# Kernel tuning notes

Measured on AMD Instinct MI355X. Metric: run time of the kernel, lower is better.

The kernel has to match this reference:

```python
import jax, jax.numpy as jnp
import numpy as np

N_NODES = 50000
N_EDGES = 800000
D_FEAT = 128


def setup_inputs() -> dict:
    key = jax.random.key(0)
    k1, k2, k3, k4 = jax.random.split(key, 4)
    edge_index = jax.random.randint(k1, (2, N_EDGES), 0, N_NODES, dtype=jnp.int64 if jax.config.jax_enable_x64 else jnp.int32)
    edge_vals = jax.random.uniform(k2, (N_EDGES,), dtype=jnp.float32)
    features = jax.random.normal(k3, (N_NODES, D_FEAT), dtype=jnp.float32)
    bias = jax.random.normal(k4, (D_FEAT,), dtype=jnp.float32)
    return {"edge_index": edge_index, "edge_vals": edge_vals, "features": features, "bias": bias}


def reference(edge_index, edge_vals, features, bias):
    # SpMM: out[dst] += A[dst, src] * X[src], i.e. sparse adjacency @ dense features
    src = edge_index[0]
    dst = edge_index[1]
    msg = features[src] * edge_vals[:, None]          # [E, D] gather + scale
    out = jax.ops.segment_sum(msg, dst, num_segments=features.shape[0])  # [N, D] scatter-add
    return out + bias                                  # fused bias add
```

## Files before the change

kernel.cpp:

```cpp
#include <hip/hip_runtime.h>
#include <hip/hip_bf16.h>

#define D_FEAT 128
#define D4 (D_FEAT / 4)
#define BKT_SHIFT 7
#define BKT_NODES 128
#define NCHUNK 256
#define MAXBKT 512
#define MAXBSUM 128
#define CAP 3072

__device__ inline unsigned pack_bf2(float lo, float hi) {
    __hip_bfloat162 h = __float22bfloat162_rn(make_float2(lo, hi));
    unsigned u;
    __builtin_memcpy(&u, &h, 4);
    return u;
}

__global__ __launch_bounds__(256) void k1_hist_cvt(
        const int* __restrict__ dst, int E, int chunk, int nbkt,
        int* __restrict__ M, int Mpad,
        const float4* __restrict__ fin, uint2* __restrict__ fout,
        int n4) {
    int c = blockIdx.x;
    int tid = threadIdx.x;
    if (c < NCHUNK) {
        __shared__ int hist[MAXBKT];
        for (int i = tid; i < nbkt; i += 256) hist[i] = 0;
        __syncthreads();
        int lo = c * chunk;
        int hi = min(lo + chunk, E);
        for (int i = lo + tid; i < hi; i += 256)
            atomicAdd(&hist[dst[i] >> BKT_SHIFT], 1);
        __syncthreads();
        for (int i = tid; i < nbkt; i += 256)
            M[i * NCHUNK + c] = hist[i];
        if (c == 0) {
            for (int i = nbkt * NCHUNK + tid; i < Mpad; i += 256) M[i] = 0;
        }
    } else {
        int nb = gridDim.x - NCHUNK;
        int idx = (c - NCHUNK) * 256 + tid;
        int stride = nb * 256;
        for (int i = idx; i < n4; i += stride) {
            float4 f = fin[i];
            uint2 o;
            o.x = pack_bf2(f.x, f.y);
            o.y = pack_bf2(f.z, f.w);
            fout[i] = o;
        }
    }
}

__global__ __launch_bounds__(1024) void k2a_scan(int* __restrict__ M,
                                                 int* __restrict__ bsum) {
    __shared__ int s[1024];
    int tid = threadIdx.x;
    int j = blockIdx.x * 1024 + tid;
    int v = M[j];
    s[tid] = v;
    __syncthreads();
    for (int off = 1; off < 1024; off <<= 1) {
        int t = (tid >= off) ? s[tid - off] : 0;
        __syncthreads();
        s[tid] += t;
        __syncthreads();
    }
    M[j] = s[tid] - v;
    if (tid == 1023) bsum[blockIdx.x] = s[1023];
}

__device__ inline void scan_bsum_wave(const int* __restrict__ bsum, int nblk,
                                      int* sbs, int tid) {
    if (tid < 64) {
        int i0 = 2 * tid, i1 = 2 * tid + 1;
        int h0 = (i0 < nblk) ? bsum[i0] : 0;
        int h1 = (i1 < nblk) ? bsum[i1] : 0;
        int s = h0 + h1;
        int v = s;
        for (int off = 1; off < 64; off <<= 1) {
            int t = __shfl_up(v, off, 64);
            if (tid >= off) v += t;
        }
        sbs[i0] = v - s;
        sbs[i1] = v - s + h0;
    }
    __syncthreads();
}

__global__ __launch_bounds__(512) void k3_partition(
        const int* __restrict__ src, const int* __restrict__ dst,
        const float* __restrict__ vals, int E, int chunk, int nbkt, int nblk,
        const int* __restrict__ M, const int* __restrict__ bsum,
        int2* __restrict__ spackA) {
    __shared__ int sbs[MAXBSUM];
    __shared__ int lcur[MAXBKT];
    int c = blockIdx.x;
    int tid = threadIdx.x;
    scan_bsum_wave(bsum, nblk, sbs, tid);
    for (int i = tid; i < nbkt; i += 512) {
        int j = i * NCHUNK + c;
        lcur[i] = M[j] + sbs[j >> 10];
    }
    __syncthreads();
    int lo = c * chunk;
    int hi = min(lo + chunk, E);
    for (int i = lo + tid; i < hi; i += 512) {
        int d = dst[i];
        int s = src[i];
        float v = vals[i];
        int pos = atomicAdd(&lcur[d >> BKT_SHIFT], 1);
        spackA[pos] = make_int2((s & 0xFFFF) | ((d & (BKT_NODES - 1)) << 16),
                                __float_as_int(v));
    }
}

__global__ __launch_bounds__(1024) void k45_sort_gather(
        const int* __restrict__ M, const int* __restrict__ bsum, int nblk,
        const int2* __restrict__ spackA, int2* __restrict__ spackB,
        const uint2* __restrict__ feat2,
        const float4* __restrict__ bias4, float4* __restrict__ out4,
        int N, int nbkt) {
    __shared__ int sbs[MAXBSUM];
    __shared__ int hist[BKT_NODES];
    __shared__ int sbuf[BKT_NODES];
    __shared__ int lcur[BKT_NODES];
    __shared__ int2 ls[CAP];
    int b = blockIdx.x;
    int tid = threadIdx.x;
    scan_bsum_wave(bsum, nblk, sbs, tid);
    int j0 = b * NCHUNK;
    int j1 = (b + 1) * NCHUNK;
    int base = M[j0] + sbs[j0 >> 10];
    int end  = M[j1] + sbs[j1 >> 10];
    int cnt = end - base;
    bool inlds = (cnt <= CAP);

    if (tid < BKT_NODES) hist[tid] = 0;
    __syncthreads();
    for (int i = tid; i < cnt; i += 1024)
        atomicAdd(&hist[(spackA[base + i].x >> 16) & (BKT_NODES - 1)], 1);
    __syncthreads();
    if (tid < 64) {
        int h0 = hist[2 * tid], h1 = hist[2 * tid + 1];
        int s = h0 + h1;
        int v = s;
        for (int off = 1; off < 64; off <<= 1) {
            int t = __shfl_up(v, off, 64);
            if (tid >= off) v += t;
        }
        sbuf[2 * tid]     = v - h1;
        sbuf[2 * tid + 1] = v;
        lcur[2 * tid]     = v - s;
        lcur[2 * tid + 1] = v - h1;
    }
    __syncthreads();
    for (int i = tid; i < cnt; i += 1024) {
        int2 r = spackA[base + i];
        int p = atomicAdd(&lcur[(r.x >> 16) & (BKT_NODES - 1)], 1);
        if (inlds) ls[p] = r;
        else       spackB[base + p] = r;
    }
    __syncthreads();

    int wave = tid >> 6, lane = tid & 63;
    int half = lane >> 5;
    int hl   = lane & 31;
    float4 bv = bias4[hl];
    for (int n = wave; n < BKT_NODES; n += 16) {
        int node = (b << BKT_SHIFT) + n;
        if (node >= N) break;
        int lend = sbuf[n];
        int lbeg = lend - hist[n];
        float4 acc0 = make_float4(0.f, 0.f, 0.f, 0.f);
        float4 acc1 = make_float4(0.f, 0.f, 0.f, 0.f);
        if (inlds) {
            for (int e0 = lbeg; e0 < lend; e0 += 16) {
                int2 p[8];
                uint2 h[8];
#pragma unroll
                for (int j = 0; j < 8; j++)
                    p[j] = ls[min(e0 + 2 * j + half, lend - 1)];
#pragma unroll
                for (int j = 0; j < 8; j++)
                    h[j] = feat2[(size_t)(p[j].x & 0xFFFF) * 32 + hl];
#pragma unroll
                for (int j = 0; j < 8; j++) {
                    float v = (e0 + 2 * j + half < lend) ? __int_as_float(p[j].y) : 0.f;
                    __hip_bfloat162 blo, bhi;
                    __builtin_memcpy(&blo, &h[j].x, 4);
                    __builtin_memcpy(&bhi, &h[j].y, 4);
                    float2 f01 = __bfloat1622float2(blo);
                    float2 f23 = __bfloat1622float2(bhi);
                    if (j & 1) {
                        acc1.x += v * f01.x; acc1.y += v * f01.y;
                        acc1.z += v * f23.x; acc1.w += v * f23.y;
                    } else {
                        acc0.x += v * f01.x; acc0.y += v * f01.y;
                        acc0.z += v * f23.x; acc0.w += v * f23.y;
                    }
                }
            }
        } else {
            for (int e0 = lbeg; e0 < lend; e0 += 16) {
                int2 p[8];
                uint2 h[8];
#pragma unroll
                for (int j = 0; j < 8; j++)
                    p[j] = spackB[base + min(e0 + 2 * j + half, lend - 1)];
#pragma unroll
                for (int j = 0; j < 8; j++)
                    h[j] = feat2[(size_t)(p[j].x & 0xFFFF) * 32 + hl];
#pragma unroll
                for (int j = 0; j < 8; j++) {
                    float v = (e0 + 2 * j + half < lend) ? __int_as_float(p[j].y) : 0.f;
                    __hip_bfloat162 blo, bhi;
                    __builtin_memcpy(&blo, &h[j].x, 4);
                    __builtin_memcpy(&bhi, &h[j].y, 4);
                    float2 f01 = __bfloat1622float2(blo);
                    float2 f23 = __bfloat1622float2(bhi);
                    if (j & 1) {
                        acc1.x += v * f01.x; acc1.y += v * f01.y;
                        acc1.z += v * f23.x; acc1.w += v * f23.y;
                    } else {
                        acc0.x += v * f01.x; acc0.y += v * f01.y;
                        acc0.z += v * f23.x; acc0.w += v * f23.y;
                    }
                }
            }
        }
        acc0.x += acc1.x; acc0.y += acc1.y;
        acc0.z += acc1.z; acc0.w += acc1.w;
        acc0.x += __shfl_xor(acc0.x, 32);
        acc0.y += __shfl_xor(acc0.y, 32);
        acc0.z += __shfl_xor(acc0.z, 32);
        acc0.w += __shfl_xor(acc0.w, 32);
        if (half == 0) {
            out4[(size_t)node * 32 + hl] =
                make_float4(acc0.x + bv.x, acc0.y + bv.y,
                            acc0.z + bv.z, acc0.w + bv.w);
        }
    }
}


__global__ void init_bias_kernel(float4* __restrict__ out,
                                 const float4* __restrict__ bias, int n4) {
    int i = blockIdx.x * blockDim.x + threadIdx.x;
    if (i < n4) out[i] = bias[i & (D4 - 1)];
}

__global__ void spmm_edge_kernel(const int* __restrict__ src,
                                 const int* __restrict__ dst,
                                 const float* __restrict__ vals,
                                 const float4* __restrict__ feat,
                                 float* __restrict__ out, int n_edges) {
    int tid = blockIdx.x * blockDim.x + threadIdx.x;
    int e = tid >> 5;
    int lane = tid & 31;
    if (e >= n_edges) return;
    int s = src[e];
    int d = dst[e];
    float v = vals[e];
    float4 f = feat[(size_t)s * D4 + lane];
    float* o = out + (size_t)d * D_FEAT + lane * 4;
    atomicAdd(o + 0, v * f.x);
    atomicAdd(o + 1, v * f.y);
    atomicAdd(o + 2, v * f.z);
    atomicAdd(o + 3, v * f.w);
}

extern "C" void kernel_launch(void* const* d_in, const int* in_sizes, int n_in,
                              void* d_out, int out_size, void* d_ws, size_t ws_size,
                              hipStream_t stream) {
    const int* edge_index = (const int*)d_in[0];
    const float* edge_vals = (const float*)d_in[1];
    const float* features  = (const float*)d_in[2];
    const float* bias      = (const float*)d_in[3];

    int E = in_sizes[1];
    int N = in_sizes[2] / D_FEAT;
    const int* src = edge_index;
    const int* dst = edge_index + E;
    float* out = (float*)d_out;

    int nbkt = (N + BKT_NODES - 1) >> BKT_SHIFT;
    int n4 = N * D_FEAT / 4;
    int chunk = (E + NCHUNK - 1) / NCHUNK;
    int Mpad = ((nbkt * NCHUNK + 1 + 1023) / 1024) * 1024;
    int nblk2 = Mpad / 1024;

    size_t fb_bytes = (size_t)N * D_FEAT * 2;
    size_t sp_bytes = (size_t)E * 8;
    size_t needed = fb_bytes + 2 * sp_bytes +
                    ((size_t)Mpad + nblk2) * 4;

    bool ok = (ws_size >= needed) && (N >= 1) && (N <= 65536) && (E >= 1) &&
              (in_sizes[3] == D_FEAT) && (nbkt <= MAXBKT) && (nblk2 <= MAXBSUM);

    if (ok) {
        char* wp = (char*)d_ws;
        uint2* fb16 = (uint2*)wp;                      wp += fb_bytes;
        int2* spackA = (int2*)wp;                      wp += sp_bytes;
        int2* spackB = (int2*)wp;                      wp += sp_bytes;
        int* M       = (int*)wp;                       wp += (size_t)Mpad * 4;
        int* bsum    = (int*)wp;

        k1_hist_cvt<<<NCHUNK + 256, 256, 0, stream>>>(dst, E, chunk, nbkt,
                                                      M, Mpad,
                                                      (const float4*)features,
                                                      fb16, n4);
        k2a_scan<<<nblk2, 1024, 0, stream>>>(M, bsum);
        k3_partition<<<NCHUNK, 512, 0, stream>>>(src, dst, edge_vals, E, chunk,
                                                 nbkt, nblk2, M, bsum, spackA);
        k45_sort_gather<<<nbkt, 1024, 0, stream>>>(M, bsum, nblk2,
                                                   spackA, spackB,
                                                   (const uint2*)fb16,
                                                   (const float4*)bias,
                                                   (float4*)out, N, nbkt);
    } else {
        int no4 = out_size / 4;
        {
            int block = 256, grid = (no4 + block - 1) / block;
            init_bias_kernel<<<grid, block, 0, stream>>>((float4*)out,
                                                         (const float4*)bias, no4);
        }
        {
            int block = 256;
            long long total = (long long)E * 32;
            int grid = (int)((total + block - 1) / block);
            spmm_edge_kernel<<<grid, block, 0, stream>>>(src, dst, edge_vals,
                                                         (const float4*)features,
                                                         out, E);
        }
    }
}
```

Baseline: 144.1 us.

## Fuse histogram, scan, partition and sort-gather into one cooperative persistent kernel

Replaces the four-kernel pipeline with a single cooperative launch that uses grid-wide syncs between the histogram/convert, scan, partition and bucket sort-gather phases. Blocks loop over chunks and buckets in a persistent style. The goal is to remove the launch gaps and tail drains between kernels. In exchange, grid size is capped by occupancy: 1024-thread blocks with large LDS use fewer blocks per CU, so phases such as the 256-chunk partition and 391-bucket gather may serialise. Grid syncs also cost time.

```diff
diff --git a/kernel.cpp b/kernel.cpp
--- a/kernel.cpp
+++ b/kernel.cpp
@@ -1,5 +1,8 @@
 #include <hip/hip_runtime.h>
 #include <hip/hip_bf16.h>
+#include <hip/hip_cooperative_groups.h>
+
+namespace cg = cooperative_groups;
 
 #define D_FEAT 128
 #define D4 (D_FEAT / 4)
@@ -15,59 +18,6 @@
     unsigned u;
     __builtin_memcpy(&u, &h, 4);
     return u;
-}
-
-__global__ __launch_bounds__(256) void k1_hist_cvt(
-        const int* __restrict__ dst, int E, int chunk, int nbkt,
-        int* __restrict__ M, int Mpad,
-        const float4* __restrict__ fin, uint2* __restrict__ fout,
-        int n4) {
-    int c = blockIdx.x;
-    int tid = threadIdx.x;
-    if (c < NCHUNK) {
-        __shared__ int hist[MAXBKT];
-        for (int i = tid; i < nbkt; i += 256) hist[i] = 0;
-        __syncthreads();
-        int lo = c * chunk;
-        int hi = min(lo + chunk, E);
-        for (int i = lo + tid; i < hi; i += 256)
-            atomicAdd(&hist[dst[i] >> BKT_SHIFT], 1);
-        __syncthreads();
-        for (int i = tid; i < nbkt; i += 256)
-            M[i * NCHUNK + c] = hist[i];
-        if (c == 0) {
-            for (int i = nbkt * NCHUNK + tid; i < Mpad; i += 256) M[i] = 0;
-        }
-    } else {
-        int nb = gridDim.x - NCHUNK;
-        int idx = (c - NCHUNK) * 256 + tid;
-        int stride = nb * 256;
-        for (int i = idx; i < n4; i += stride) {
-            float4 f = fin[i];
-            uint2 o;
-            o.x = pack_bf2(f.x, f.y);
-            o.y = pack_bf2(f.z, f.w);
-            fout[i] = o;
-        }
-    }
-}
-
-__global__ __launch_bounds__(1024) void k2a_scan(int* __restrict__ M,
-                                                 int* __restrict__ bsum) {
-    __shared__ int s[1024];
-    int tid = threadIdx.x;
-    int j = blockIdx.x * 1024 + tid;
-    int v = M[j];
-    s[tid] = v;
-    __syncthreads();
-    for (int off = 1; off < 1024; off <<= 1) {
-        int t = (tid >= off) ? s[tid - off] : 0;
-        __syncthreads();
-        s[tid] += t;
-        __syncthreads();
-    }
-    M[j] = s[tid] - v;
-    if (tid == 1023) bsum[blockIdx.x] = s[1023];
 }
 
 __device__ inline void scan_bsum_wave(const int* __restrict__ bsum, int nblk,
@@ -86,6 +36,260 @@
         sbs[i1] = v - s + h0;
     }
     __syncthreads();
+}
+
+__global__ __launch_bounds__(1024) void fused_all(
+        const int* __restrict__ src, const int* __restrict__ dst,
+        const float* __restrict__ vals, int E, int chunk,
+        int nbkt, int Mpad, int nblk2,
+        int* __restrict__ M, int* __restrict__ bsum,
+        int2* __restrict__ spackA, int2* __restrict__ spackB,
+        const float4* __restrict__ fin4, uint2* __restrict__ fb16, int n4,
+        const float4* __restrict__ bias4, float4* __restrict__ out4, int N) {
+    cg::grid_group grid = cg::this_grid();
+    __shared__ int sh_hist[MAXBKT];
+    __shared__ int sh_scan[1024];
+    __shared__ int sbs[MAXBSUM];
+    __shared__ int lcur[MAXBKT];
+    __shared__ int h4[BKT_NODES];
+    __shared__ int sb4[BKT_NODES];
+    __shared__ int lc4[BKT_NODES];
+    __shared__ int2 ls[CAP];
+    int b = blockIdx.x;
+    int tid = threadIdx.x;
+    int G = gridDim.x;
+
+    for (int c = b; c < NCHUNK; c += G) {
+        for (int i = tid; i < nbkt; i += 1024) sh_hist[i] = 0;
+        __syncthreads();
+        int lo = c * chunk;
+        int hi = min(lo + chunk, E);
+        for (int i = lo + tid; i < hi; i += 1024)
+            atomicAdd(&sh_hist[dst[i] >> BKT_SHIFT], 1);
+        __syncthreads();
+        for (int i = tid; i < nbkt; i += 1024) M[i * NCHUNK + c] = sh_hist[i];
+        __syncthreads();
+    }
+    {
+        int g0 = b * 1024 + tid;
+        for (int i = nbkt * NCHUNK + g0; i < Mpad; i += G * 1024) M[i] = 0;
+        for (int i = g0; i < n4; i += G * 1024) {
+            float4 f = fin4[i];
+            uint2 o;
+            o.x = pack_bf2(f.x, f.y);
+            o.y = pack_bf2(f.z, f.w);
+            fb16[i] = o;
+        }
+    }
+    grid.sync();
+
+    for (int blk = b; blk < nblk2; blk += G) {
+        int j = blk * 1024 + tid;
+        int v = M[j];
+        sh_scan[tid] = v;
+        __syncthreads();
+        for (int off = 1; off < 1024; off <<= 1) {
+            int t = (tid >= off) ? sh_scan[tid - off] : 0;
+            __syncthreads();
+            sh_scan[tid] += t;
+            __syncthreads();
+        }
+        M[j] = sh_scan[tid] - v;
+        if (tid == 1023) bsum[blk] = sh_scan[1023];
+        __syncthreads();
+    }
+    grid.sync();
+
+    scan_bsum_wave(bsum, nblk2, sbs, tid);
+    for (int c = b; c < NCHUNK; c += G) {
+        for (int i = tid; i < nbkt; i += 1024) {
+            int j = i * NCHUNK + c;
+            lcur[i] = M[j] + sbs[j >> 10];
+        }
+        __syncthreads();
+        int lo = c * chunk;
+        int hi = min(lo + chunk, E);
+        for (int i = lo + tid; i < hi; i += 1024) {
+            int d = dst[i];
+            int pos = atomicAdd(&lcur[d >> BKT_SHIFT], 1);
+            spackA[pos] = make_int2((src[i] & 0xFFFF) |
+                                    ((d & (BKT_NODES - 1)) << 16),
+                                    __float_as_int(vals[i]));
+        }
+        __syncthreads();
+    }
+    grid.sync();
+
+    for (int bk = b; bk < nbkt; bk += G) {
+        int j0 = bk * NCHUNK;
+        int j1 = (bk + 1) * NCHUNK;
+        int base = M[j0] + sbs[j0 >> 10];
+        int end  = M[j1] + sbs[j1 >> 10];
+        int cnt = end - base;
+        bool inlds = (cnt <= CAP);
+
+        if (tid < BKT_NODES) h4[tid] = 0;
+        __syncthreads();
+        for (int i = tid; i < cnt; i += 1024)
+            atomicAdd(&h4[(spackA[base + i].x >> 16) & (BKT_NODES - 1)], 1);
+        __syncthreads();
+        if (tid < 64) {
+            int h0 = h4[2 * tid], h1 = h4[2 * tid + 1];
+            int s = h0 + h1;
+            int v = s;
+            for (int off = 1; off < 64; off <<= 1) {
+                int t = __shfl_up(v, off, 64);
+                if (tid >= off) v += t;
+            }
+            sb4[2 * tid]     = v - h1;
+            sb4[2 * tid + 1] = v;
+            lc4[2 * tid]     = v - s;
+            lc4[2 * tid + 1] = v - h1;
+        }
+        __syncthreads();
+        for (int i = tid; i < cnt; i += 1024) {
+            int2 r = spackA[base + i];
+            int p = atomicAdd(&lc4[(r.x >> 16) & (BKT_NODES - 1)], 1);
+            if (inlds) ls[p] = r;
+            else       spackB[base + p] = r;
+        }
+        __syncthreads();
+
+        int wave = tid >> 6, lane = tid & 63;
+        int half = lane >> 5;
+        int hl   = lane & 31;
+        float4 bv = bias4[hl];
+        for (int n = wave; n < BKT_NODES; n += 16) {
+            int node = (bk << BKT_SHIFT) + n;
+            if (node >= N) break;
+            int lend = sb4[n];
+            int lbeg = lend - h4[n];
+            float4 a0 = make_float4(0.f, 0.f, 0.f, 0.f);
+            float4 a1 = make_float4(0.f, 0.f, 0.f, 0.f);
+            if (inlds) {
+                for (int e0 = lbeg; e0 < lend; e0 += 16) {
+                    int2 p[8];
+                    uint2 h[8];
+#pragma unroll
+                    for (int j = 0; j < 8; j++)
+                        p[j] = ls[min(e0 + 2 * j + half, lend - 1)];
+#pragma unroll
+                    for (int j = 0; j < 8; j++)
+                        h[j] = fb16[(size_t)(p[j].x & 0xFFFF) * 32 + hl];
+#pragma unroll
+                    for (int j = 0; j < 8; j++) {
+                        float v = (e0 + 2 * j + half < lend) ?
+                                  __int_as_float(p[j].y) : 0.f;
+                        __hip_bfloat162 blo, bhi;
+                        __builtin_memcpy(&blo, &h[j].x, 4);
+                        __builtin_memcpy(&bhi, &h[j].y, 4);
+                        float2 f01 = __bfloat1622float2(blo);
+                        float2 f23 = __bfloat1622float2(bhi);
+                        if (j & 1) {
+                            a1.x += v * f01.x; a1.y += v * f01.y;
+                            a1.z += v * f23.x; a1.w += v * f23.y;
+                        } else {
+                            a0.x += v * f01.x; a0.y += v * f01.y;
+                            a0.z += v * f23.x; a0.w += v * f23.y;
+                        }
+                    }
+                }
+            } else {
+                for (int e0 = lbeg; e0 < lend; e0 += 16) {
+                    int2 p[8];
+                    uint2 h[8];
+#pragma unroll
+                    for (int j = 0; j < 8; j++)
+                        p[j] = spackB[base + min(e0 + 2 * j + half, lend - 1)];
+#pragma unroll
+                    for (int j = 0; j < 8; j++)
+                        h[j] = fb16[(size_t)(p[j].x & 0xFFFF) * 32 + hl];
+#pragma unroll
+                    for (int j = 0; j < 8; j++) {
+                        float v = (e0 + 2 * j + half < lend) ?
+                                  __int_as_float(p[j].y) : 0.f;
+                        __hip_bfloat162 blo, bhi;
+                        __builtin_memcpy(&blo, &h[j].x, 4);
+                        __builtin_memcpy(&bhi, &h[j].y, 4);
+                        float2 f01 = __bfloat1622float2(blo);
+                        float2 f23 = __bfloat1622float2(bhi);
+                        if (j & 1) {
+                            a1.x += v * f01.x; a1.y += v * f01.y;
+                            a1.z += v * f23.x; a1.w += v * f23.y;
+                        } else {
+                            a0.x += v * f01.x; a0.y += v * f01.y;
+                            a0.z += v * f23.x; a0.w += v * f23.y;
+                        }
+                    }
+                }
+            }
+            a0.x += a1.x; a0.y += a1.y; a0.z += a1.z; a0.w += a1.w;
+            a0.x += __shfl_xor(a0.x, 32);
+            a0.y += __shfl_xor(a0.y, 32);
+            a0.z += __shfl_xor(a0.z, 32);
+            a0.w += __shfl_xor(a0.w, 32);
+            if (half == 0) {
+                out4[(size_t)node * 32 + hl] =
+                    make_float4(a0.x + bv.x, a0.y + bv.y,
+                                a0.z + bv.z, a0.w + bv.w);
+            }
+        }
+        __syncthreads();
+    }
+}
+
+
+__global__ __launch_bounds__(256) void k1_hist_cvt(
+        const int* __restrict__ dst, int E, int chunk, int nbkt,
+        int* __restrict__ M, int Mpad,
+        const float4* __restrict__ fin, uint2* __restrict__ fout,
+        int n4) {
+    int c = blockIdx.x;
+    int tid = threadIdx.x;
+    if (c < NCHUNK) {
+        __shared__ int hist[MAXBKT];
+        for (int i = tid; i < nbkt; i += 256) hist[i] = 0;
+        __syncthreads();
+        int lo = c * chunk;
+        int hi = min(lo + chunk, E);
+        for (int i = lo + tid; i < hi; i += 256)
+            atomicAdd(&hist[dst[i] >> BKT_SHIFT], 1);
+        __syncthreads();
+        for (int i = tid; i < nbkt; i += 256)
+            M[i * NCHUNK + c] = hist[i];
+        if (c == 0) {
+            for (int i = nbkt * NCHUNK + tid; i < Mpad; i += 256) M[i] = 0;
+        }
+    } else {
+        int nb = gridDim.x - NCHUNK;
+        int idx = (c - NCHUNK) * 256 + tid;
+        int stride = nb * 256;
+        for (int i = idx; i < n4; i += stride) {
+            float4 f = fin[i];
+            uint2 o;
+            o.x = pack_bf2(f.x, f.y);
+            o.y = pack_bf2(f.z, f.w);
+            fout[i] = o;
+        }
+    }
+}
+
+__global__ __launch_bounds__(1024) void k2a_scan(int* __restrict__ M,
+                                                 int* __restrict__ bsum) {
+    __shared__ int s[1024];
+    int tid = threadIdx.x;
+    int j = blockIdx.x * 1024 + tid;
+    int v = M[j];
+    s[tid] = v;
+    __syncthreads();
+    for (int off = 1; off < 1024; off <<= 1) {
+        int t = (tid >= off) ? s[tid - off] : 0;
+        __syncthreads();
+        s[tid] += t;
+        __syncthreads();
+    }
+    M[j] = s[tid] - v;
+    if (tid == 1023) bsum[blockIdx.x] = s[1023];
 }
 
 __global__ __launch_bounds__(512) void k3_partition(
@@ -107,11 +311,9 @@
     int hi = min(lo + chunk, E);
     for (int i = lo + tid; i < hi; i += 512) {
         int d = dst[i];
-        int s = src[i];
-        float v = vals[i];
         int pos = atomicAdd(&lcur[d >> BKT_SHIFT], 1);
-        spackA[pos] = make_int2((s & 0xFFFF) | ((d & (BKT_NODES - 1)) << 16),
-                                __float_as_int(v));
+        spackA[pos] = make_int2((src[i] & 0xFFFF) | ((d & (BKT_NODES - 1)) << 16),
+                                __float_as_int(vals[i]));
     }
 }
 
@@ -172,8 +374,8 @@
         if (node >= N) break;
         int lend = sbuf[n];
         int lbeg = lend - hist[n];
-        float4 acc0 = make_float4(0.f, 0.f, 0.f, 0.f);
-        float4 acc1 = make_float4(0.f, 0.f, 0.f, 0.f);
+        float4 a0 = make_float4(0.f, 0.f, 0.f, 0.f);
+        float4 a1 = make_float4(0.f, 0.f, 0.f, 0.f);
         if (inlds) {
             for (int e0 = lbeg; e0 < lend; e0 += 16) {
                 int2 p[8];
@@ -193,11 +395,11 @@
                     float2 f01 = __bfloat1622float2(blo);
                     float2 f23 = __bfloat1622float2(bhi);
                     if (j & 1) {
-                        acc1.x += v * f01.x; acc1.y += v * f01.y;
-                        acc1.z += v * f23.x; acc1.w += v * f23.y;
+                        a1.x += v * f01.x; a1.y += v * f01.y;
+                        a1.z += v * f23.x; a1.w += v * f23.y;
                     } else {
-                        acc0.x += v * f01.x; acc0.y += v * f01.y;
-                        acc0.z += v * f23.x; acc0.w += v * f23.y;
+                        a0.x += v * f01.x; a0.y += v * f01.y;
+                        a0.z += v * f23.x; a0.w += v * f23.y;
                     }
                 }
             }
@@ -220,25 +422,24 @@
                     float2 f01 = __bfloat1622float2(blo);
                     float2 f23 = __bfloat1622float2(bhi);
                     if (j & 1) {
-                        acc1.x += v * f01.x; acc1.y += v * f01.y;
-                        acc1.z += v * f23.x; acc1.w += v * f23.y;
+                        a1.x += v * f01.x; a1.y += v * f01.y;
+                        a1.z += v * f23.x; a1.w += v * f23.y;
                     } else {
-                        acc0.x += v * f01.x; acc0.y += v * f01.y;
-                        acc0.z += v * f23.x; acc0.w += v * f23.y;
+                        a0.x += v * f01.x; a0.y += v * f01.y;
+                        a0.z += v * f23.x; a0.w += v * f23.y;
                     }
                 }
             }
         }
-        acc0.x += acc1.x; acc0.y += acc1.y;
-        acc0.z += acc1.z; acc0.w += acc1.w;
-        acc0.x += __shfl_xor(acc0.x, 32);
-        acc0.y += __shfl_xor(acc0.y, 32);
-        acc0.z += __shfl_xor(acc0.z, 32);
-        acc0.w += __shfl_xor(acc0.w, 32);
+        a0.x += a1.x; a0.y += a1.y; a0.z += a1.z; a0.w += a1.w;
+        a0.x += __shfl_xor(a0.x, 32);
+        a0.y += __shfl_xor(a0.y, 32);
+        a0.z += __shfl_xor(a0.z, 32);
+        a0.w += __shfl_xor(a0.w, 32);
         if (half == 0) {
             out4[(size_t)node * 32 + hl] =
-                make_float4(acc0.x + bv.x, acc0.y + bv.y,
-                            acc0.z + bv.z, acc0.w + bv.w);
+                make_float4(a0.x + bv.x, a0.y + bv.y,
+                            a0.z + bv.z, a0.w + bv.w);
         }
     }
 }
@@ -292,8 +493,7 @@
 
     size_t fb_bytes = (size_t)N * D_FEAT * 2;
     size_t sp_bytes = (size_t)E * 8;
-    size_t needed = fb_bytes + 2 * sp_bytes +
-                    ((size_t)Mpad + nblk2) * 4;
+    size_t needed = fb_bytes + 2 * sp_bytes + ((size_t)Mpad + nblk2) * 4;
 
     bool ok = (ws_size >= needed) && (N >= 1) && (N <= 65536) && (E >= 1) &&
               (in_sizes[3] == D_FEAT) && (nbkt <= MAXBKT) && (nblk2 <= MAXBSUM);
@@ -306,18 +506,53 @@
         int* M       = (int*)wp;                       wp += (size_t)Mpad * 4;
         int* bsum    = (int*)wp;
 
-        k1_hist_cvt<<<NCHUNK + 256, 256, 0, stream>>>(dst, E, chunk, nbkt,
-                                                      M, Mpad,
-                                                      (const float4*)features,
-                                                      fb16, n4);
-        k2a_scan<<<nblk2, 1024, 0, stream>>>(M, bsum);
-        k3_partition<<<NCHUNK, 512, 0, stream>>>(src, dst, edge_vals, E, chunk,
-                                                 nbkt, nblk2, M, bsum, spackA);
-        k45_sort_gather<<<nbkt, 1024, 0, stream>>>(M, bsum, nblk2,
-                                                   spackA, spackB,
-                                                   (const uint2*)fb16,
-                                                   (const float4*)bias,
-                                                   (float4*)out, N, nbkt);
+        static int s_cap = -2;
+        if (s_cap == -2) {
+            int nb = 0;
+            if (hipOccupancyMaxActiveBlocksPerMultiprocessor(
+                    &nb, fused_all, 1024, 0) != hipSuccess) nb = 0;
+            int cus = 0;
+            hipDeviceProp_t prop;
+            int dev = 0;
+            if (hipGetDevice(&dev) == hipSuccess &&
+                hipGetDeviceProperties(&prop, dev) == hipSuccess)
+                cus = prop.multiProcessorCount;
+            s_cap = (nb > 0 && cus > 0) ? nb * cus : 0;
+        }
+
+        bool launched = false;
+        if (s_cap >= 64) {
+            int G = s_cap < 512 ? s_cap : 512;
+            const float4* fin4 = (const float4*)features;
+            const float4* bias4 = (const float4*)bias;
+            float4* out4 = (float4*)out;
+            void* args[] = {
+                (void*)&src, (void*)&dst, (void*)&edge_vals, (void*)&E,
+                (void*)&chunk, (void*)&nbkt, (void*)&Mpad, (void*)&nblk2,
+                (void*)&M, (void*)&bsum, (void*)&spackA, (void*)&spackB,
+                (void*)&fin4, (void*)&fb16, (void*)&n4,
+                (void*)&bias4, (void*)&out4, (void*)&N };
+            hipError_t err = hipLaunchCooperativeKernel(
+                fused_all, dim3(G), dim3(1024), args, 0, stream);
+            if (err == hipSuccess) launched = true;
+            else s_cap = 0;
+        }
+
+        if (!launched) {
+            k1_hist_cvt<<<NCHUNK + 256, 256, 0, stream>>>(dst, E, chunk, nbkt,
+                                                          M, Mpad,
+                                                          (const float4*)features,
+                                                          fb16, n4);
+            k2a_scan<<<nblk2, 1024, 0, stream>>>(M, bsum);
+            k3_partition<<<NCHUNK, 512, 0, stream>>>(src, dst, edge_vals, E,
+                                                     chunk, nbkt, nblk2,
+                                                     M, bsum, spackA);
+            k45_sort_gather<<<nbkt, 1024, 0, stream>>>(M, bsum, nblk2,
+                                                       spackA, spackB,
+                                                       (const uint2*)fb16,
+                                                       (const float4*)bias,
+                                                       (float4*)out, N, nbkt);
+        }
     } else {
         int no4 = out_size / 4;
         {
```

Result: no change. 142.5 us (-1.1%).

## Replace scan-based partition with fixed bucket slots and an overflow path

Applied to the files above, without the earlier changes.

Drops the global histogram matrix, its prefix-scan kernel and the separate partition pass. Each chunk now reserves space in a fixed-size per-bucket slot with a global atomic cursor and scatters edges in the same kernel as the bf16 conversion, which cuts the launch count and removes one full pass over dst. Edges that overflow a slot go to a side list, and a separate kernel adds them into the output with fp32 atomics. This adds a memset, a third launch that always runs, and nondeterministic atomic ordering for overflowed edges.

```diff
diff --git a/kernel.cpp b/kernel.cpp
--- a/kernel.cpp
+++ b/kernel.cpp
@@ -7,8 +7,7 @@
 #define BKT_NODES 128
 #define NCHUNK 256
 #define MAXBKT 512
-#define MAXBSUM 128
-#define CAP 3072
+#define SLOT 5120
 
 __device__ inline unsigned pack_bf2(float lo, float hi) {
     __hip_bfloat162 h = __float22bfloat162_rn(make_float2(lo, hi));
@@ -17,124 +16,71 @@
     return u;
 }
 
-__global__ __launch_bounds__(256) void k1_hist_cvt(
-        const int* __restrict__ dst, int E, int chunk, int nbkt,
-        int* __restrict__ M, int Mpad,
-        const float4* __restrict__ fin, uint2* __restrict__ fout,
-        int n4) {
+__global__ __launch_bounds__(512) void ka_part_cvt(
+        const int* __restrict__ src, const int* __restrict__ dst,
+        const float* __restrict__ vals, int E, int chunk, int nbkt,
+        int* __restrict__ gcur, int* __restrict__ ovcnt, int4* __restrict__ ov,
+        int2* __restrict__ spackA,
+        const float4* __restrict__ fin4, uint2* __restrict__ fb16, int n4) {
     int c = blockIdx.x;
     int tid = threadIdx.x;
     if (c < NCHUNK) {
         __shared__ int hist[MAXBKT];
-        for (int i = tid; i < nbkt; i += 256) hist[i] = 0;
+        __shared__ int lcur[MAXBKT];
+        for (int i = tid; i < nbkt; i += 512) hist[i] = 0;
         __syncthreads();
         int lo = c * chunk;
         int hi = min(lo + chunk, E);
-        for (int i = lo + tid; i < hi; i += 256)
+        for (int i = lo + tid; i < hi; i += 512)
             atomicAdd(&hist[dst[i] >> BKT_SHIFT], 1);
         __syncthreads();
-        for (int i = tid; i < nbkt; i += 256)
-            M[i * NCHUNK + c] = hist[i];
-        if (c == 0) {
-            for (int i = nbkt * NCHUNK + tid; i < Mpad; i += 256) M[i] = 0;
+        for (int i = tid; i < nbkt; i += 512) {
+            int h = hist[i];
+            lcur[i] = h ? (i * SLOT + atomicAdd(&gcur[i], h)) : 0;
+        }
+        __syncthreads();
+        for (int i = lo + tid; i < hi; i += 512) {
+            int d = dst[i];
+            int s = src[i];
+            float v = vals[i];
+            int bkt = d >> BKT_SHIFT;
+            int pos = atomicAdd(&lcur[bkt], 1);
+            if (pos - bkt * SLOT < SLOT) {
+                spackA[pos] = make_int2((s & 0xFFFF) |
+                                        ((d & (BKT_NODES - 1)) << 16),
+                                        __float_as_int(v));
+            } else {
+                int oi = atomicAdd(ovcnt, 1);
+                ov[oi] = make_int4(s, d, __float_as_int(v), 0);
+            }
         }
     } else {
         int nb = gridDim.x - NCHUNK;
-        int idx = (c - NCHUNK) * 256 + tid;
-        int stride = nb * 256;
+        int idx = (c - NCHUNK) * 512 + tid;
+        int stride = nb * 512;
         for (int i = idx; i < n4; i += stride) {
-            float4 f = fin[i];
+            float4 f = fin4[i];
             uint2 o;
             o.x = pack_bf2(f.x, f.y);
             o.y = pack_bf2(f.z, f.w);
-            fout[i] = o;
-        }
-    }
-}
-
-__global__ __launch_bounds__(1024) void k2a_scan(int* __restrict__ M,
-                                                 int* __restrict__ bsum) {
-    __shared__ int s[1024];
-    int tid = threadIdx.x;
-    int j = blockIdx.x * 1024 + tid;
-    int v = M[j];
-    s[tid] = v;
-    __syncthreads();
-    for (int off = 1; off < 1024; off <<= 1) {
-        int t = (tid >= off) ? s[tid - off] : 0;
-        __syncthreads();
-        s[tid] += t;
-        __syncthreads();
-    }
-    M[j] = s[tid] - v;
-    if (tid == 1023) bsum[blockIdx.x] = s[1023];
-}
-
-__device__ inline void scan_bsum_wave(const int* __restrict__ bsum, int nblk,
-                                      int* sbs, int tid) {
-    if (tid < 64) {
-        int i0 = 2 * tid, i1 = 2 * tid + 1;
-        int h0 = (i0 < nblk) ? bsum[i0] : 0;
-        int h1 = (i1 < nblk) ? bsum[i1] : 0;
-        int s = h0 + h1;
-        int v = s;
-        for (int off = 1; off < 64; off <<= 1) {
-            int t = __shfl_up(v, off, 64);
-            if (tid >= off) v += t;
-        }
-        sbs[i0] = v - s;
-        sbs[i1] = v - s + h0;
-    }
-    __syncthreads();
-}
-
-__global__ __launch_bounds__(512) void k3_partition(
-        const int* __restrict__ src, const int* __restrict__ dst,
-        const float* __restrict__ vals, int E, int chunk, int nbkt, int nblk,
-        const int* __restrict__ M, const int* __restrict__ bsum,
-        int2* __restrict__ spackA) {
-    __shared__ int sbs[MAXBSUM];
-    __shared__ int lcur[MAXBKT];
-    int c = blockIdx.x;
-    int tid = threadIdx.x;
-    scan_bsum_wave(bsum, nblk, sbs, tid);
-    for (int i = tid; i < nbkt; i += 512) {
-        int j = i * NCHUNK + c;
-        lcur[i] = M[j] + sbs[j >> 10];
-    }
-    __syncthreads();
-    int lo = c * chunk;
-    int hi = min(lo + chunk, E);
-    for (int i = lo + tid; i < hi; i += 512) {
-        int d = dst[i];
-        int s = src[i];
-        float v = vals[i];
-        int pos = atomicAdd(&lcur[d >> BKT_SHIFT], 1);
-        spackA[pos] = make_int2((s & 0xFFFF) | ((d & (BKT_NODES - 1)) << 16),
-                                __float_as_int(v));
-    }
-}
-
-__global__ __launch_bounds__(1024) void k45_sort_gather(
-        const int* __restrict__ M, const int* __restrict__ bsum, int nblk,
-        const int2* __restrict__ spackA, int2* __restrict__ spackB,
+            fb16[i] = o;
+        }
+    }
+}
+
+__global__ __launch_bounds__(1024) void kb_sort_gather(
+        const int* __restrict__ gcur, const int2* __restrict__ spackA,
         const uint2* __restrict__ feat2,
-        const float4* __restrict__ bias4, float4* __restrict__ out4,
-        int N, int nbkt) {
-    __shared__ int sbs[MAXBSUM];
+        const float4* __restrict__ bias4, float4* __restrict__ out4, int N) {
     __shared__ int hist[BKT_NODES];
     __shared__ int sbuf[BKT_NODES];
     __shared__ int lcur[BKT_NODES];
-    __shared__ int2 ls[CAP];
+    __shared__ int2 ls[SLOT];
     int b = blockIdx.x;
     int tid = threadIdx.x;
-    scan_bsum_wave(bsum, nblk, sbs, tid);
-    int j0 = b * NCHUNK;
-    int j1 = (b + 1) * NCHUNK;
-    int base = M[j0] + sbs[j0 >> 10];
-    int end  = M[j1] + sbs[j1 >> 10];
-    int cnt = end - base;
-    bool inlds = (cnt <= CAP);
+    int cnt = gcur[b];
+    if (cnt > SLOT) cnt = SLOT;
+    int base = b * SLOT;
 
     if (tid < BKT_NODES) hist[tid] = 0;
     __syncthreads();
@@ -158,8 +104,7 @@
     for (int i = tid; i < cnt; i += 1024) {
         int2 r = spackA[base + i];
         int p = atomicAdd(&lcur[(r.x >> 16) & (BKT_NODES - 1)], 1);
-        if (inlds) ls[p] = r;
-        else       spackB[base + p] = r;
+        ls[p] = r;
     }
     __syncthreads();
 
@@ -172,74 +117,66 @@
         if (node >= N) break;
         int lend = sbuf[n];
         int lbeg = lend - hist[n];
-        float4 acc0 = make_float4(0.f, 0.f, 0.f, 0.f);
-        float4 acc1 = make_float4(0.f, 0.f, 0.f, 0.f);
-        if (inlds) {
-            for (int e0 = lbeg; e0 < lend; e0 += 16) {
-                int2 p[8];
-                uint2 h[8];
+        float4 a0 = make_float4(0.f, 0.f, 0.f, 0.f);
+        float4 a1 = make_float4(0.f, 0.f, 0.f, 0.f);
+        for (int e0 = lbeg; e0 < lend; e0 += 16) {
+            int2 p[8];
+            uint2 h[8];
 #pragma unroll
-                for (int j = 0; j < 8; j++)
-                    p[j] = ls[min(e0 + 2 * j + half, lend - 1)];
+            for (int j = 0; j < 8; j++)
+                p[j] = ls[min(e0 + 2 * j + half, lend - 1)];
 #pragma unroll
-                for (int j = 0; j < 8; j++)
-                    h[j] = feat2[(size_t)(p[j].x & 0xFFFF) * 32 + hl];
+            for (int j = 0; j < 8; j++)
+                h[j] = feat2[(size_t)(p[j].x & 0xFFFF) * 32 + hl];
 #pragma unroll
-                for (int j = 0; j < 8; j++) {
-                    float v = (e0 + 2 * j + half < lend) ? __int_as_float(p[j].y) : 0.f;
-                    __hip_bfloat162 blo, bhi;
-                    __builtin_memcpy(&blo, &h[j].x, 4);
-                    __builtin_memcpy(&bhi, &h[j].y, 4);
-                    float2 f01 = __bfloat1622float2(blo);
-                    float2 f23 = __bfloat1622float2(bhi);
-                    if (j & 1) {
-                        acc1.x += v * f01.x; acc1.y += v * f01.y;
-                        acc1.z += v * f23.x; acc1.w += v * f23.y;
-                    } else {
-                        acc0.x += v * f01.x; acc0.y += v * f01.y;
-                        acc0.z += v * f23.x; acc0.w += v * f23.y;
-                    }
+            for (int j = 0; j < 8; j++) {
+                float v = (e0 + 2 * j + half < lend) ?
+                          __int_as_float(p[j].y) : 0.f;
+                __hip_bfloat162 blo, bhi;
+                __builtin_memcpy(&blo, &h[j].x, 4);
+                __builtin_memcpy(&bhi, &h[j].y, 4);
+                float2 f01 = __bfloat1622float2(blo);
+                float2 f23 = __bfloat1622float2(bhi);
+                if (j & 1) {
+                    a1.x += v * f01.x; a1.y += v * f01.y;
+                    a1.z += v * f23.x; a1.w += v * f23.y;
+                } else {
+                    a0.x += v * f01.x; a0.y += v * f01.y;
+                    a0.z += v * f23.x; a0.w += v * f23.y;
                 }
             }
-        } else {
-            for (int e0 = lbeg; e0 < lend; e0 += 16) {
-                int2 p[8];
-                uint2 h[8];
-#pragma unroll
-                for (int j = 0; j < 8; j++)
-                    p[j] = spackB[base + min(e0 + 2 * j + half, lend - 1)];
-#pragma unroll
-                for (int j = 0; j < 8; j++)
-                    h[j] = feat2[(size_t)(p[j].x & 0xFFFF) * 32 + hl];
-#pragma unroll
-                for (int j = 0; j < 8; j++) {
-                    float v = (e0 + 2 * j + half < lend) ? __int_as_float(p[j].y) : 0.f;
-                    __hip_bfloat162 blo, bhi;
-                    __builtin_memcpy(&blo, &h[j].x, 4);
-                    __builtin_memcpy(&bhi, &h[j].y, 4);
-                    float2 f01 = __bfloat1622float2(blo);
-                    float2 f23 = __bfloat1622float2(bhi);
-                    if (j & 1) {
-                        acc1.x += v * f01.x; acc1.y += v * f01.y;
-                        acc1.z += v * f23.x; acc1.w += v * f23.y;
-                    } else {
-                        acc0.x += v * f01.x; acc0.y += v * f01.y;
-                        acc0.z += v * f23.x; acc0.w += v * f23.y;
-                    }
-                }
-            }
-        }
-        acc0.x += acc1.x; acc0.y += acc1.y;
-        acc0.z += acc1.z; acc0.w += acc1.w;
-        acc0.x += __shfl_xor(acc0.x, 32);
-        acc0.y += __shfl_xor(acc0.y, 32);
-        acc0.z += __shfl_xor(acc0.z, 32);
-        acc0.w += __shfl_xor(acc0.w, 32);
+        }
+        a0.x += a1.x; a0.y += a1.y; a0.z += a1.z; a0.w += a1.w;
+        a0.x += __shfl_xor(a0.x, 32);
+        a0.y += __shfl_xor(a0.y, 32);
+        a0.z += __shfl_xor(a0.z, 32);
+        a0.w += __shfl_xor(a0.w, 32);
         if (half == 0) {
             out4[(size_t)node * 32 + hl] =
-                make_float4(acc0.x + bv.x, acc0.y + bv.y,
-                            acc0.z + bv.z, acc0.w + bv.w);
-        }
+                make_float4(a0.x + bv.x, a0.y + bv.y,
+                            a0.z + bv.z, a0.w + bv.w);
+        }
+    }
+}
+
+__global__ __launch_bounds__(256) void k_over(
+        const int4* __restrict__ ov, const int* __restrict__ ovcnt,
+        const float4* __restrict__ feat4, float* __restrict__ out) {
+    int total = *ovcnt;
+    long long items = (long long)total * 32;
+    long long stride = (long long)gridDim.x * blockDim.x;
+    for (long long i = (long long)blockIdx.x * blockDim.x + threadIdx.x;
+         i < items; i += stride) {
+        int e = (int)(i >> 5);
+        int lane = (int)(i & 31);
+        int4 r = ov[e];
+        float v = __int_as_float(r.z);
+        float4 f = feat4[(size_t)r.x * 32 + lane];
+        float* o = out + (size_t)r.y * D_FEAT + lane * 4;
+        atomicAdd(o + 0, v * f.x);
+        atomicAdd(o + 1, v * f.y);
+        atomicAdd(o + 2, v * f.z);
+        atomicAdd(o + 3, v * f.w);
     }
 }
 
@@ -287,37 +224,34 @@
     int nbkt = (N + BKT_NODES - 1) >> BKT_SHIFT;
     int n4 = N * D_FEAT / 4;
     int chunk = (E + NCHUNK - 1) / NCHUNK;
-    int Mpad = ((nbkt * NCHUNK + 1 + 1023) / 1024) * 1024;
-    int nblk2 = Mpad / 1024;
 
     size_t fb_bytes = (size_t)N * D_FEAT * 2;
-    size_t sp_bytes = (size_t)E * 8;
-    size_t needed = fb_bytes + 2 * sp_bytes +
-                    ((size_t)Mpad + nblk2) * 4;
+    size_t spA_bytes = (size_t)nbkt * SLOT * 8;
+    size_t ov_bytes = (size_t)E * 16;
+    size_t needed = fb_bytes + spA_bytes + ov_bytes + ((size_t)MAXBKT + 1) * 4;
 
     bool ok = (ws_size >= needed) && (N >= 1) && (N <= 65536) && (E >= 1) &&
-              (in_sizes[3] == D_FEAT) && (nbkt <= MAXBKT) && (nblk2 <= MAXBSUM);
+              (in_sizes[3] == D_FEAT) && (nbkt <= MAXBKT);
 
     if (ok) {
         char* wp = (char*)d_ws;
         uint2* fb16 = (uint2*)wp;                      wp += fb_bytes;
-        int2* spackA = (int2*)wp;                      wp += sp_bytes;
-        int2* spackB = (int2*)wp;                      wp += sp_bytes;
-        int* M       = (int*)wp;                       wp += (size_t)Mpad * 4;
-        int* bsum    = (int*)wp;
-
-        k1_hist_cvt<<<NCHUNK + 256, 256, 0, stream>>>(dst, E, chunk, nbkt,
-                                                      M, Mpad,
-                                                      (const float4*)features,
-                                                      fb16, n4);
-        k2a_scan<<<nblk2, 1024, 0, stream>>>(M, bsum);
-        k3_partition<<<NCHUNK, 512, 0, stream>>>(src, dst, edge_vals, E, chunk,
-                                                 nbkt, nblk2, M, bsum, spackA);
-        k45_sort_gather<<<nbkt, 1024, 0, stream>>>(M, bsum, nblk2,
-                                                   spackA, spackB,
-                                                   (const uint2*)fb16,
-                                                   (const float4*)bias,
-                                                   (float4*)out, N, nbkt);
+        int2* spackA = (int2*)wp;                      wp += spA_bytes;
+        int4* ov     = (int4*)wp;                      wp += ov_bytes;
+        int* gcur    = (int*)wp;
+        int* ovcnt   = gcur + MAXBKT;
+
+        hipMemsetAsync(gcur, 0, ((size_t)MAXBKT + 1) * 4, stream);
+
+        ka_part_cvt<<<NCHUNK + 256, 512, 0, stream>>>(
+            src, dst, edge_vals, E, chunk, nbkt,
+            gcur, ovcnt, ov, spackA,
+            (const float4*)features, fb16, n4);
+        kb_sort_gather<<<nbkt, 1024, 0, stream>>>(
+            gcur, spackA, (const uint2*)fb16,
+            (const float4*)bias, (float4*)out, N);
+        k_over<<<128, 256, 0, stream>>>(ov, ovcnt,
+                                        (const float4*)features, out);
     } else {
         int no4 = out_size / 4;
         {
```

New measurement: 139.1 us. -3.5%, faster.
